# Kernel optimization log

Measured on AMD Instinct MI355X. Metric: run time of the kernel, lower is better.

## Reference

```python
import jax, jax.numpy as jnp
import numpy as np

DECAY = 0.99
EPS = 1e-05


def setup_inputs() -> dict:
    key = jax.random.key(0)
    k1, k2 = jax.random.split(key)
    N, D, K = 262144, 32, 1024
    z = jax.random.normal(k1, (N, D), dtype=jnp.float32)
    # xavier_normal_ on (K, D): std = sqrt(2 / (K + D))
    std = float(np.sqrt(2.0 / (K + D)))
    embedding = jax.random.normal(k2, (K, D), dtype=jnp.float32) * std
    embed_avg = embedding  # buffer initialized as a clone of the codebook
    cluster_size = jnp.ones((K,), dtype=jnp.float32)
    return {"z": z, "embedding": embedding, "embed_avg": embed_avg,
            "cluster_size": cluster_size}


def reference(z, embedding, embed_avg, cluster_size):
    n_embed, embed_dim = embedding.shape
    # squared euclidean cdist: ||z||^2 + ||e||^2 - 2 z e^T  -> [N, K]
    d = (jnp.sum(z * z, axis=1, keepdims=True)
         + jnp.sum(embedding * embedding, axis=1)
         - 2.0 * (z @ embedding.T))
    encoding_indices = jnp.argmin(d, axis=1)  # [N]
    # one-hot column sums via scatter-add (counts per code)
    counts = jnp.zeros((n_embed,), z.dtype).at[encoding_indices].add(1.0)
    unused_codes = jnp.sum(counts == 0)
    # embedding gather
    z_q = embedding[encoding_indices]  # [N, D]
    # EMA scatter-add update (training branch, use_ema=True)
    embed_sum = jnp.zeros_like(embedding).at[encoding_indices].add(z)  # [K, D]
    cluster_size_new = DECAY * cluster_size + (1.0 - DECAY) * counts
    embed_avg_new = DECAY * embed_avg + (1.0 - DECAY) * embed_sum
    n = jnp.sum(cluster_size_new)
    norm_w = n * (cluster_size_new + EPS) / (n + n_embed * EPS)  # Laplace smoothing
    embedding_new = embed_avg_new / norm_w[:, None]
    codebook_loss = jnp.float32(0.0)
    commitment_loss = jnp.mean((z - jax.lax.stop_gradient(z_q)) ** 2)
    # straight-through estimator
    z_q_out = z + jax.lax.stop_gradient(z_q - z)
    return (z_q_out, codebook_loss, commitment_loss, encoding_indices,
            unused_codes, embedding_new, cluster_size_new, embed_avg_new)
```

## Files before the change

### kernel.cpp

```cpp
#include <hip/hip_runtime.h>
#include <hip/hip_bf16.h>
#include <float.h>

#define DIM 32
#define KCODES 1024
#define NROWS 262144
#define NBLK 256

#define O_ZQ   0
#define O_CB   8388608
#define O_CL   8388609
#define O_IDX  8388610
#define O_UN   8650754
#define O_EMB  8650755
#define O_CS   8683523
#define O_EA   8684547

#define W_PCNT 0
#define W_PSUM 262144
#define W_PCOM 8650752
#define W_NORM 8651008
#define W_ZZH  8652032
#define W_EEH  8914176
#define W_BF   8915200

typedef __attribute__((ext_vector_type(8))) short bf16x8;
typedef __attribute__((ext_vector_type(4))) float f32x4;
typedef __attribute__((ext_vector_type(4))) int i32x4;

#define MFMA16 __builtin_amdgcn_mfma_f32_16x16x32_bf16

static __device__ __forceinline__ unsigned short f2bf(float x) {
    __hip_bfloat16 h = __float2bfloat16(x);
    return __builtin_bit_cast(unsigned short, h);
}
static __device__ __forceinline__ float bf2f(unsigned short u) {
    unsigned int v = ((unsigned int)u) << 16;
    return __builtin_bit_cast(float, v);
}
static __device__ __forceinline__ float pw8_sq(const float* x) {
    float w[32];
    #pragma unroll
    for (int i = 0; i < 32; ++i) w[i] = __fmul_rn(x[i], x[i]);
    float r[8];
    #pragma unroll
    for (int j = 0; j < 8; ++j) r[j] = ((w[j] + w[8 + j]) + w[16 + j]) + w[24 + j];
    return ((r[0] + r[1]) + (r[2] + r[3])) + ((r[4] + r[5]) + (r[6] + r[7]));
}

__global__ __launch_bounds__(256) void vq_prep_z(
    const float* __restrict__ z, float* __restrict__ ws)
{
    int row = blockIdx.x * 256 + threadIdx.x;
    float x[32];
    const float4* zg = (const float4*)(z + (size_t)row * DIM);
    #pragma unroll
    for (int q = 0; q < 8; ++q) {
        float4 v = zg[q];
        x[4*q] = v.x; x[4*q+1] = v.y; x[4*q+2] = v.z; x[4*q+3] = v.w;
    }
    ws[W_ZZH + row] = 0.5f * pw8_sq(x);
}

__global__ __launch_bounds__(256) void vq_prep_e(
    const float* __restrict__ emb, float* __restrict__ ws)
{
    int c = blockIdx.x * 256 + threadIdx.x;
    float x[32];
    const float4* eg = (const float4*)(emb + (size_t)c * DIM);
    #pragma unroll
    for (int q = 0; q < 8; ++q) {
        float4 v = eg[q];
        x[4*q] = v.x; x[4*q+1] = v.y; x[4*q+2] = v.z; x[4*q+3] = v.w;
    }
    ws[W_EEH + c] = 0.5f * pw8_sq(x);

    unsigned short hb[3][32];
    #pragma unroll
    for (int i = 0; i < 32; ++i) {
        float v = x[i];
        unsigned short h0 = f2bf(v); float f0 = bf2f(h0); float r1 = v - f0;
        unsigned short h1 = f2bf(r1); float f1 = bf2f(h1); float r2 = r1 - f1;
        unsigned short h2 = f2bf(r2);
        hb[0][i] = h0; hb[1][i] = h1; hb[2][i] = h2;
    }
    bf16x8* bf = (bf16x8*)(ws + W_BF);
    int ct = c >> 4, cl = c & 15;
    #pragma unroll
    for (int s = 0; s < 3; ++s) {
        #pragma unroll
        for (int j = 0; j < 4; ++j) {
            bf16x8 pk;
            #pragma unroll
            for (int e = 0; e < 8; ++e) pk[e] = (short)hb[s][j*8 + e];
            bf[(ct*3 + s)*64 + j*16 + cl] = pk;
        }
    }
}

__global__ __launch_bounds__(512) void vq_argmin_mfma(
    const float* __restrict__ z, const float* __restrict__ wsc,
    float* __restrict__ out)
{
    __shared__ unsigned short bsh[49152];
    __shared__ float eesh[1024];
    const int t = threadIdx.x;
    const int lane = t & 63, w = t >> 6;
    const int g = lane >> 4, lr = lane & 15;

    const unsigned short* bfG = (const unsigned short*)(wsc + W_BF);
    const float* zzh = wsc + W_ZZH;

    for (int i = t; i < 1024; i += 512) eesh[i] = wsc[W_EEH + i];

    const int rtbase = blockIdx.x * 64 + w * 8;

    for (int pair = 0; pair < 4; ++pair) {
        const int rt0 = rtbase + pair * 2;
        const int rt1 = rt0 + 1;
        bf16x8 zh0, zm0, zl0, zh1, zm1, zl1;
        float4 zz0, zz1;
        {
            const float* zp0 = z + ((size_t)(rt0*16 + lr))*DIM + g*8;
            const float* zp1 = z + ((size_t)(rt1*16 + lr))*DIM + g*8;
            float4 a0 = *(const float4*)zp0, b0 = *(const float4*)(zp0+4);
            float4 a1 = *(const float4*)zp1, b1 = *(const float4*)(zp1+4);
            float xs0[8] = {a0.x,a0.y,a0.z,a0.w,b0.x,b0.y,b0.z,b0.w};
            float xs1[8] = {a1.x,a1.y,a1.z,a1.w,b1.x,b1.y,b1.z,b1.w};
            #pragma unroll
            for (int e = 0; e < 8; ++e) {
                float v = xs0[e];
                unsigned short h0 = f2bf(v); float f0 = bf2f(h0); float r1 = v - f0;
                unsigned short h1 = f2bf(r1); float f1 = bf2f(h1); float r2 = r1 - f1;
                zh0[e] = (short)h0; zm0[e] = (short)h1; zl0[e] = (short)f2bf(r2);
            }
            #pragma unroll
            for (int e = 0; e < 8; ++e) {
                float v = xs1[e];
                unsigned short h0 = f2bf(v); float f0 = bf2f(h0); float r1 = v - f0;
                unsigned short h1 = f2bf(r1); float f1 = bf2f(h1); float r2 = r1 - f1;
                zh1[e] = (short)h0; zm1[e] = (short)h1; zl1[e] = (short)f2bf(r2);
            }
            zz0 = *(const float4*)(zzh + rt0*16 + g*4);
            zz1 = *(const float4*)(zzh + rt1*16 + g*4);
        }
        float zza0[4] = {zz0.x, zz0.y, zz0.z, zz0.w};
        float zza1[4] = {zz1.x, zz1.y, zz1.z, zz1.w};

        unsigned int Bb0[4], Bb1[4]; int Kk0[4], Kk1[4];
        #pragma unroll
        for (int r = 0; r < 4; ++r) { Bb0[r] = 0xFFFFFFFFu; Bb1[r] = 0xFFFFFFFFu; Kk0[r] = 0; Kk1[r] = 0; }

        for (int half = 0; half < 2; ++half) {
            __syncthreads();
            {
                const i32x4* src = (const i32x4*)(bfG + half * 49152);
                i32x4* dst = (i32x4*)bsh;
                #pragma unroll
                for (int i = 0; i < 12; ++i) dst[t + i*512] = src[t + i*512];
            }
            __syncthreads();
            const bf16x8* bv = (const bf16x8*)bsh;
            for (int ct = 0; ct < 32; ++ct) {
                bf16x8 eh = bv[(ct*3 + 0)*64 + lane];
                bf16x8 em = bv[(ct*3 + 1)*64 + lane];
                bf16x8 el = bv[(ct*3 + 2)*64 + lane];
                float ee_l = eesh[(half*32 + ct)*16 + lr];
                int kge = (half*32 + ct)*16 + lr;
                f32x4 a0 = {0.f,0.f,0.f,0.f}, a1 = {0.f,0.f,0.f,0.f};
                a0 = MFMA16(zh0, eh, a0, 0,0,0);  a1 = MFMA16(zh1, eh, a1, 0,0,0);
                a0 = MFMA16(zh0, em, a0, 0,0,0);  a1 = MFMA16(zh1, em, a1, 0,0,0);
                a0 = MFMA16(zm0, eh, a0, 0,0,0);  a1 = MFMA16(zm1, eh, a1, 0,0,0);
                a0 = MFMA16(zh0, el, a0, 0,0,0);  a1 = MFMA16(zh1, el, a1, 0,0,0);
                a0 = MFMA16(zl0, eh, a0, 0,0,0);  a1 = MFMA16(zl1, eh, a1, 0,0,0);
                a0 = MFMA16(zm0, em, a0, 0,0,0);  a1 = MFMA16(zm1, em, a1, 0,0,0);
                #pragma unroll
                for (int r = 0; r < 4; ++r) {
                    float v0 = (zza0[r] + ee_l) - a0[r];
                    float v1 = (zza1[r] + ee_l) - a1[r];
                    unsigned int u0 = __builtin_bit_cast(unsigned int, v0);
                    unsigned int u1 = __builtin_bit_cast(unsigned int, v1);
                    bool t0 = u0 < Bb0[r];  Bb0[r] = t0 ? u0 : Bb0[r];  Kk0[r] = t0 ? kge : Kk0[r];
                    bool t1 = u1 < Bb1[r];  Bb1[r] = t1 ? u1 : Bb1[r];  Kk1[r] = t1 ? kge : Kk1[r];
                }
            }
        }
        #pragma unroll
        for (int r = 0; r < 4; ++r) {
            unsigned int b0 = Bb0[r]; int k0 = Kk0[r];
            unsigned int b1 = Bb1[r]; int k1 = Kk1[r];
            #pragma unroll
            for (int m = 1; m < 16; m <<= 1) {
                unsigned int ob = __shfl_xor((int)b0, m, 16); int ok = __shfl_xor(k0, m, 16);
                bool tk = (ob < b0) || (ob == b0 && ok < k0);
                b0 = tk ? ob : b0; k0 = tk ? ok : k0;
                unsigned int pb = __shfl_xor((int)b1, m, 16); int pk = __shfl_xor(k1, m, 16);
                bool tq = (pb < b1) || (pb == b1 && pk < k1);
                b1 = tq ? pb : b1; k1 = tq ? pk : k1;
            }
            if (lr == 0) {
                out[O_IDX + rt0*16 + g*4 + r] = (float)k0;
                out[O_IDX + rt1*16 + g*4 + r] = (float)k1;
            }
        }
    }
}

__global__ __launch_bounds__(1024) void vq_scatter(
    const float* __restrict__ z, const float* __restrict__ emb,
    float* __restrict__ out, float* __restrict__ ws)
{
    __shared__ float smem[34816];
    __shared__ float red[16];
    const int t = threadIdx.x;
    const int b = blockIdx.x;
    #pragma unroll
    for (int i = 0; i < 33; ++i) smem[t * 33 + i] = 0.f;
    smem[33792 + t] = 0.f;
    __syncthreads();

    const int row = b * 1024 + t;
    const int kk = (int)out[O_IDX + row];
    const float4* zg = (const float4*)(z + (size_t)row * DIM);
    const float4* eg = (const float4*)(emb + (size_t)kk * DIM);
    float4* og = (float4*)(out + O_ZQ + (size_t)row * DIM);
    float zv[32];
    float csum = 0.f;
    #pragma unroll
    for (int q = 0; q < 8; ++q) {
        float4 v = zg[q];
        float4 e = eg[q];
        zv[4*q] = v.x; zv[4*q+1] = v.y; zv[4*q+2] = v.z; zv[4*q+3] = v.w;
        float d0 = v.x - e.x, d1 = v.y - e.y, d2 = v.z - e.z, d3 = v.w - e.w;
        csum = fmaf(d0, d0, csum); csum = fmaf(d1, d1, csum);
        csum = fmaf(d2, d2, csum); csum = fmaf(d3, d3, csum);
        float4 o;
        o.x = v.x + (e.x - v.x); o.y = v.y + (e.y - v.y);
        o.z = v.z + (e.z - v.z); o.w = v.w + (e.w - v.w);
        og[q] = o;
    }
    atomicAdd(&smem[33792 + kk], 1.0f);
    #pragma unroll
    for (int i = 0; i < 32; ++i) atomicAdd(&smem[kk * 33 + i], zv[i]);

    #pragma unroll
    for (int off = 32; off > 0; off >>= 1) csum += __shfl_down(csum, off, 64);
    if ((t & 63) == 0) red[t >> 6] = csum;
    __syncthreads();

    ws[W_PCNT + b * KCODES + t] = smem[33792 + t];
    float4* p4 = (float4*)(ws + W_PSUM + (size_t)b * (KCODES * DIM));
    #pragma unroll
    for (int c = 0; c < 8; ++c) {
        int j = t + c * 1024;
        int kr = j >> 3, e0 = (j & 7) * 4;
        float4 v;
        v.x = smem[kr * 33 + e0 + 0]; v.y = smem[kr * 33 + e0 + 1];
        v.z = smem[kr * 33 + e0 + 2]; v.w = smem[kr * 33 + e0 + 3];
        p4[j] = v;
    }
    if (t == 0) {
        float s = 0.f;
        #pragma unroll
        for (int i = 0; i < 16; ++i) s += red[i];
        ws[W_PCOM + b] = s;
    }
}

__global__ __launch_bounds__(1024) void vq_epilogue0(
    const float* __restrict__ cs_in, const float* __restrict__ ws,
    float* __restrict__ out, float* __restrict__ wsw)
{
    __shared__ float s1[1024], s2[1024];
    const int k = threadIdx.x;
    float c = 0.f;
    for (int bb = 0; bb < NBLK; ++bb) c += ws[W_PCNT + bb * KCODES + k];
    float csn = 0.99f * cs_in[k] + 0.01f * c;
    out[O_CS + k] = csn;
    s1[k] = csn;
    s2[k] = (c == 0.f) ? 1.f : 0.f;
    __syncthreads();
    for (int s = 512; s > 0; s >>= 1) {
        if (k < s) { s1[k] += s1[k + s]; s2[k] += s2[k + s]; }
        __syncthreads();
    }
    float n = s1[0];
    float unused = s2[0];
    wsw[W_NORM + k] = n * (csn + 1e-5f) / (n + 1024.f * 1e-5f);
    __syncthreads();
    s1[k] = (k < NBLK) ? ws[W_PCOM + k] : 0.f;
    __syncthreads();
    for (int s = 512; s > 0; s >>= 1) {
        if (k < s) s1[k] += s1[k + s];
        __syncthreads();
    }
    if (k == 0) {
        out[O_CB] = 0.f;
        out[O_CL] = s1[0] / 8388608.f;
        out[O_UN] = unused;
    }
}

__global__ void vq_epilogue1(
    const float* __restrict__ ea, const float* __restrict__ ws,
    float* __restrict__ out)
{
    const int id = blockIdx.x * 128 + threadIdx.x;
    float es = 0.f;
    for (int bb = 0; bb < NBLK; ++bb) es += ws[W_PSUM + (size_t)bb * (KCODES * DIM) + id];
    float ean = 0.99f * ea[id] + 0.01f * es;
    out[O_EA + id] = ean;
    out[O_EMB + id] = ean / ws[W_NORM + (id >> 5)];
}

extern "C" void kernel_launch(void* const* d_in, const int* in_sizes, int n_in,
                              void* d_out, int out_size, void* d_ws, size_t ws_size,
                              hipStream_t stream)
{
    const float* z   = (const float*)d_in[0];
    const float* emb = (const float*)d_in[1];
    const float* ea  = (const float*)d_in[2];
    const float* cs  = (const float*)d_in[3];
    float* out = (float*)d_out;
    float* ws  = (float*)d_ws;

    vq_prep_z<<<1024, 256, 0, stream>>>(z, ws);
    vq_prep_e<<<4, 256, 0, stream>>>(emb, ws);
    vq_argmin_mfma<<<NBLK, 512, 0, stream>>>(z, ws, out);
    vq_scatter<<<NBLK, 1024, 0, stream>>>(z, emb, out, ws);
    vq_epilogue0<<<1, 1024, 0, stream>>>(cs, ws, out, ws);
    vq_epilogue1<<<NBLK, 128, 0, stream>>>(ea, ws, out);
}
```

Before: 185.0 us.

## Double-buffer codebook tiles via async LDS loads and hold four row tiles per wave

The argmin kernel now streams the bf16-split codebook in eight chunks into a double-buffered shared-memory area, using global_load_lds. The next chunk loads while MFMAs run on the current one. Each wave now keeps four row tiles in registers and reuses every codebook fragment across them, and the grid grows to 512 blocks with half the rows per block. The scatter kernel zeroes shared memory with float4 stores and accumulates counts with global atomics instead of per-block partials, which removes the 256-way count reduction in the epilogue and needs a memset up front. The risks are higher register pressure and LDS-staging correctness with only a single barrier per chunk.

New measurement: 215.4 us. 16.4% more time.

```diff
diff --git a/kernel.cpp b/kernel.cpp
--- a/kernel.cpp
+++ b/kernel.cpp
@@ -5,7 +5,6 @@
 #define DIM 32
 #define KCODES 1024
 #define NROWS 262144
-#define NBLK 256
 
 #define O_ZQ   0
 #define O_CB   8388608
@@ -26,7 +25,6 @@
 
 typedef __attribute__((ext_vector_type(8))) short bf16x8;
 typedef __attribute__((ext_vector_type(4))) float f32x4;
-typedef __attribute__((ext_vector_type(4))) int i32x4;
 
 #define MFMA16 __builtin_amdgcn_mfma_f32_16x16x32_bf16
 
@@ -102,108 +100,104 @@
     const float* __restrict__ z, const float* __restrict__ wsc,
     float* __restrict__ out)
 {
-    __shared__ unsigned short bsh[49152];
+    __shared__ unsigned short bsh[2][12288];
     __shared__ float eesh[1024];
     const int t = threadIdx.x;
     const int lane = t & 63, w = t >> 6;
     const int g = lane >> 4, lr = lane & 15;
 
     const unsigned short* bfG = (const unsigned short*)(wsc + W_BF);
-    const float* zzh = wsc + W_ZZH;
-
-    for (int i = t; i < 1024; i += 512) eesh[i] = wsc[W_EEH + i];
-
-    const int rtbase = blockIdx.x * 64 + w * 8;
-
-    for (int pair = 0; pair < 4; ++pair) {
-        const int rt0 = rtbase + pair * 2;
-        const int rt1 = rt0 + 1;
-        bf16x8 zh0, zm0, zl0, zh1, zm1, zl1;
-        float4 zz0, zz1;
-        {
-            const float* zp0 = z + ((size_t)(rt0*16 + lr))*DIM + g*8;
-            const float* zp1 = z + ((size_t)(rt1*16 + lr))*DIM + g*8;
-            float4 a0 = *(const float4*)zp0, b0 = *(const float4*)(zp0+4);
-            float4 a1 = *(const float4*)zp1, b1 = *(const float4*)(zp1+4);
-            float xs0[8] = {a0.x,a0.y,a0.z,a0.w,b0.x,b0.y,b0.z,b0.w};
-            float xs1[8] = {a1.x,a1.y,a1.z,a1.w,b1.x,b1.y,b1.z,b1.w};
+
+    eesh[t] = wsc[W_EEH + t];
+    eesh[t + 512] = wsc[W_EEH + t + 512];
+
+#define STAGE(cc, bufi) { \
+    const char* src_ = (const char*)bfG + (size_t)(cc) * 24576; \
+    _Pragma("unroll") for (int i_ = 0; i_ < 3; ++i_) { \
+        int slot_ = i_ * 512 + w * 64; \
+        __builtin_amdgcn_global_load_lds( \
+            (const __attribute__((address_space(1))) unsigned int*)(src_ + (size_t)(slot_ + lane) * 16), \
+            (__attribute__((address_space(3))) unsigned int*)((char*)&bsh[bufi][0] + slot_ * 16), \
+            16, 0, 0); } }
+
+    const int rtbase = blockIdx.x * 32 + w * 4;
+    bf16x8 zh[4], zm[4], zl[4];
+    float zza[4][4];
+    #pragma unroll
+    for (int j = 0; j < 4; ++j) {
+        const int rtg = rtbase + j;
+        const float* zp = z + ((size_t)(rtg * 16 + lr)) * DIM + g * 8;
+        float4 a4 = *(const float4*)zp, b4 = *(const float4*)(zp + 4);
+        float xs[8] = {a4.x, a4.y, a4.z, a4.w, b4.x, b4.y, b4.z, b4.w};
+        #pragma unroll
+        for (int e = 0; e < 8; ++e) {
+            float v = xs[e];
+            unsigned short h0 = f2bf(v); float f0 = bf2f(h0); float r1 = v - f0;
+            unsigned short h1 = f2bf(r1); float f1 = bf2f(h1); float r2 = r1 - f1;
+            zh[j][e] = (short)h0; zm[j][e] = (short)h1; zl[j][e] = (short)f2bf(r2);
+        }
+        float4 zv = *(const float4*)(wsc + W_ZZH + rtg * 16 + g * 4);
+        zza[j][0] = zv.x; zza[j][1] = zv.y; zza[j][2] = zv.z; zza[j][3] = zv.w;
+    }
+
+    unsigned int Bb[4][4]; int Kk[4][4];
+    #pragma unroll
+    for (int j = 0; j < 4; ++j)
+        #pragma unroll
+        for (int r = 0; r < 4; ++r) { Bb[j][r] = 0xFFFFFFFFu; Kk[j][r] = 0; }
+
+    STAGE(0, 0)
+    __syncthreads();
+
+    for (int c = 0; c < 8; ++c) {
+        if (c < 7) STAGE(c + 1, (c + 1) & 1)
+        const bf16x8* bv = (const bf16x8*)&bsh[c & 1][0];
+        #pragma unroll
+        for (int ct = 0; ct < 8; ++ct) {
+            const int kt = c * 8 + ct;
+            bf16x8 eh = bv[(ct * 3 + 0) * 64 + lane];
+            bf16x8 em = bv[(ct * 3 + 1) * 64 + lane];
+            bf16x8 el = bv[(ct * 3 + 2) * 64 + lane];
+            float ee_l = eesh[kt * 16 + lr];
+            int kge = kt * 16 + lr;
             #pragma unroll
-            for (int e = 0; e < 8; ++e) {
-                float v = xs0[e];
-                unsigned short h0 = f2bf(v); float f0 = bf2f(h0); float r1 = v - f0;
-                unsigned short h1 = f2bf(r1); float f1 = bf2f(h1); float r2 = r1 - f1;
-                zh0[e] = (short)h0; zm0[e] = (short)h1; zl0[e] = (short)f2bf(r2);
-            }
-            #pragma unroll
-            for (int e = 0; e < 8; ++e) {
-                float v = xs1[e];
-                unsigned short h0 = f2bf(v); float f0 = bf2f(h0); float r1 = v - f0;
-                unsigned short h1 = f2bf(r1); float f1 = bf2f(h1); float r2 = r1 - f1;
-                zh1[e] = (short)h0; zm1[e] = (short)h1; zl1[e] = (short)f2bf(r2);
-            }
-            zz0 = *(const float4*)(zzh + rt0*16 + g*4);
-            zz1 = *(const float4*)(zzh + rt1*16 + g*4);
-        }
-        float zza0[4] = {zz0.x, zz0.y, zz0.z, zz0.w};
-        float zza1[4] = {zz1.x, zz1.y, zz1.z, zz1.w};
-
-        unsigned int Bb0[4], Bb1[4]; int Kk0[4], Kk1[4];
-        #pragma unroll
-        for (int r = 0; r < 4; ++r) { Bb0[r] = 0xFFFFFFFFu; Bb1[r] = 0xFFFFFFFFu; Kk0[r] = 0; Kk1[r] = 0; }
-
-        for (int half = 0; half < 2; ++half) {
-            __syncthreads();
-            {
-                const i32x4* src = (const i32x4*)(bfG + half * 49152);
-                i32x4* dst = (i32x4*)bsh;
-                #pragma unroll
-                for (int i = 0; i < 12; ++i) dst[t + i*512] = src[t + i*512];
-            }
-            __syncthreads();
-            const bf16x8* bv = (const bf16x8*)bsh;
-            for (int ct = 0; ct < 32; ++ct) {
-                bf16x8 eh = bv[(ct*3 + 0)*64 + lane];
-                bf16x8 em = bv[(ct*3 + 1)*64 + lane];
-                bf16x8 el = bv[(ct*3 + 2)*64 + lane];
-                float ee_l = eesh[(half*32 + ct)*16 + lr];
-                int kge = (half*32 + ct)*16 + lr;
-                f32x4 a0 = {0.f,0.f,0.f,0.f}, a1 = {0.f,0.f,0.f,0.f};
-                a0 = MFMA16(zh0, eh, a0, 0,0,0);  a1 = MFMA16(zh1, eh, a1, 0,0,0);
-                a0 = MFMA16(zh0, em, a0, 0,0,0);  a1 = MFMA16(zh1, em, a1, 0,0,0);
-                a0 = MFMA16(zm0, eh, a0, 0,0,0);  a1 = MFMA16(zm1, eh, a1, 0,0,0);
-                a0 = MFMA16(zh0, el, a0, 0,0,0);  a1 = MFMA16(zh1, el, a1, 0,0,0);
-                a0 = MFMA16(zl0, eh, a0, 0,0,0);  a1 = MFMA16(zl1, eh, a1, 0,0,0);
-                a0 = MFMA16(zm0, em, a0, 0,0,0);  a1 = MFMA16(zm1, em, a1, 0,0,0);
+            for (int j = 0; j < 4; ++j) {
+                f32x4 a = {0.f, 0.f, 0.f, 0.f};
+                a = MFMA16(zh[j], eh, a, 0, 0, 0);
+                a = MFMA16(zh[j], em, a, 0, 0, 0);
+                a = MFMA16(zm[j], eh, a, 0, 0, 0);
+                a = MFMA16(zh[j], el, a, 0, 0, 0);
+                a = MFMA16(zl[j], eh, a, 0, 0, 0);
+                a = MFMA16(zm[j], em, a, 0, 0, 0);
                 #pragma unroll
                 for (int r = 0; r < 4; ++r) {
-                    float v0 = (zza0[r] + ee_l) - a0[r];
-                    float v1 = (zza1[r] + ee_l) - a1[r];
-                    unsigned int u0 = __builtin_bit_cast(unsigned int, v0);
-                    unsigned int u1 = __builtin_bit_cast(unsigned int, v1);
-                    bool t0 = u0 < Bb0[r];  Bb0[r] = t0 ? u0 : Bb0[r];  Kk0[r] = t0 ? kge : Kk0[r];
-                    bool t1 = u1 < Bb1[r];  Bb1[r] = t1 ? u1 : Bb1[r];  Kk1[r] = t1 ? kge : Kk1[r];
+                    float v = (zza[j][r] + ee_l) - a[r];
+                    unsigned int u = __builtin_bit_cast(unsigned int, v);
+                    bool tk = u < Bb[j][r];
+                    Bb[j][r] = tk ? u : Bb[j][r];
+                    Kk[j][r] = tk ? kge : Kk[j][r];
                 }
             }
         }
+        __syncthreads();
+    }
+
+    #pragma unroll
+    for (int j = 0; j < 4; ++j) {
+        const int rtg = rtbase + j;
         #pragma unroll
         for (int r = 0; r < 4; ++r) {
-            unsigned int b0 = Bb0[r]; int k0 = Kk0[r];
-            unsigned int b1 = Bb1[r]; int k1 = Kk1[r];
+            unsigned int b0 = Bb[j][r]; int k0 = Kk[j][r];
             #pragma unroll
             for (int m = 1; m < 16; m <<= 1) {
                 unsigned int ob = __shfl_xor((int)b0, m, 16); int ok = __shfl_xor(k0, m, 16);
                 bool tk = (ob < b0) || (ob == b0 && ok < k0);
                 b0 = tk ? ob : b0; k0 = tk ? ok : k0;
-                unsigned int pb = __shfl_xor((int)b1, m, 16); int pk = __shfl_xor(k1, m, 16);
-                bool tq = (pb < b1) || (pb == b1 && pk < k1);
-                b1 = tq ? pb : b1; k1 = tq ? pk : k1;
             }
-            if (lr == 0) {
-                out[O_IDX + rt0*16 + g*4 + r] = (float)k0;
-                out[O_IDX + rt1*16 + g*4 + r] = (float)k1;
-            }
+            if (lr == 0) out[O_IDX + rtg * 16 + g * 4 + r] = (float)k0;
         }
     }
+#undef STAGE
 }
 
 __global__ __launch_bounds__(1024) void vq_scatter(
@@ -214,9 +208,12 @@
     __shared__ float red[16];
     const int t = threadIdx.x;
     const int b = blockIdx.x;
-    #pragma unroll
-    for (int i = 0; i < 33; ++i) smem[t * 33 + i] = 0.f;
-    smem[33792 + t] = 0.f;
+    {
+        float4 zero4 = {0.f, 0.f, 0.f, 0.f};
+        float4* s4 = (float4*)smem;
+        #pragma unroll
+        for (int i = 0; i < 9; ++i) { int j = t + i * 1024; if (j < 8704) s4[j] = zero4; }
+    }
     __syncthreads();
 
     const int row = b * 1024 + t;
@@ -248,7 +245,9 @@
     if ((t & 63) == 0) red[t >> 6] = csum;
     __syncthreads();
 
-    ws[W_PCNT + b * KCODES + t] = smem[33792 + t];
+    float cpart = smem[33792 + t];
+    if (cpart != 0.f) atomicAdd(&ws[W_PCNT + t], cpart);
+
     float4* p4 = (float4*)(ws + W_PSUM + (size_t)b * (KCODES * DIM));
     #pragma unroll
     for (int c = 0; c < 8; ++c) {
@@ -273,8 +272,7 @@
 {
     __shared__ float s1[1024], s2[1024];
     const int k = threadIdx.x;
-    float c = 0.f;
-    for (int bb = 0; bb < NBLK; ++bb) c += ws[W_PCNT + bb * KCODES + k];
+    float c = ws[W_PCNT + k];
     float csn = 0.99f * cs_in[k] + 0.01f * c;
     out[O_CS + k] = csn;
     s1[k] = csn;
@@ -288,7 +286,7 @@
     float unused = s2[0];
     wsw[W_NORM + k] = n * (csn + 1e-5f) / (n + 1024.f * 1e-5f);
     __syncthreads();
-    s1[k] = (k < NBLK) ? ws[W_PCOM + k] : 0.f;
+    s1[k] = (k < 256) ? ws[W_PCOM + k] : 0.f;
     __syncthreads();
     for (int s = 512; s > 0; s >>= 1) {
         if (k < s) s1[k] += s1[k + s];
@@ -307,7 +305,7 @@
 {
     const int id = blockIdx.x * 128 + threadIdx.x;
     float es = 0.f;
-    for (int bb = 0; bb < NBLK; ++bb) es += ws[W_PSUM + (size_t)bb * (KCODES * DIM) + id];
+    for (int bb = 0; bb < 256; ++bb) es += ws[W_PSUM + (size_t)bb * (KCODES * DIM) + id];
     float ean = 0.99f * ea[id] + 0.01f * es;
     out[O_EA + id] = ean;
     out[O_EMB + id] = ean / ws[W_NORM + (id >> 5)];
@@ -324,10 +322,11 @@
     float* out = (float*)d_out;
     float* ws  = (float*)d_ws;
 
+    hipMemsetAsync(ws + W_PCNT, 0, KCODES * sizeof(float), stream);
     vq_prep_z<<<1024, 256, 0, stream>>>(z, ws);
     vq_prep_e<<<4, 256, 0, stream>>>(emb, ws);
-    vq_argmin_mfma<<<NBLK, 512, 0, stream>>>(z, ws, out);
-    vq_scatter<<<NBLK, 1024, 0, stream>>>(z, emb, out, ws);
+    vq_argmin_mfma<<<512, 512, 0, stream>>>(z, ws, out);
+    vq_scatter<<<256, 1024, 0, stream>>>(z, emb, out, ws);
     vq_epilogue0<<<1, 1024, 0, stream>>>(cs, ws, out, ws);
-    vq_epilogue1<<<NBLK, 128, 0, stream>>>(ea, ws, out);
-}
+    vq_epilogue1<<<256, 128, 0, stream>>>(ea, ws, out);
+}
```
